# Performance work log

Measured on AMD Instinct MI355X. Metric: run time of the kernel, lower is better.

## Reference

```python
import jax, jax.numpy as jnp
import numpy as np

BN_EPS = 1e-5


def setup_inputs() -> dict:
    key = jax.random.key(0)
    k1, k2, k3 = jax.random.split(key, 3)
    B, C, H, W = 8, 1024, 48, 48
    Cb = 512
    x = jax.random.normal(k1, (B, C, H, W), dtype=jnp.float32)
    Wg = jax.random.normal(k2, (Cb, C), dtype=jnp.float32) * (1.0 / np.sqrt(C))
    Wz = jax.random.normal(k3, (C, Cb), dtype=jnp.float32) * (1.0 / np.sqrt(Cb))
    gamma = jnp.zeros((C,), dtype=jnp.float32)  # BN weight, const-init 0
    beta = jnp.zeros((C,), dtype=jnp.float32)   # BN bias,  const-init 0
    return {"x": x, "Wg": Wg, "Wz": Wz, "gamma": gamma, "beta": beta}


def reference(x, Wg, Wz, gamma, beta):
    B, C, H, W = x.shape
    HW = H * W
    xf = x.reshape(B, C, HW)                                  # [B,C,N]
    # attn[b,n,m] = <x[b,:,n], x[b,:,m]> / (H*W), softmax over m
    attn = jnp.einsum('bcn,bcm->bnm', xf, xf) / HW            # [B,N,N]
    attn = jax.nn.softmax(attn, axis=-1)
    # g: 1x1 conv C -> Cb (no bias)
    g = jnp.einsum('dc,bcn->bdn', Wg, xf)                     # [B,Cb,N]
    # y[b,d,n] = sum_m attn[b,n,m] * g[b,d,m]
    y = jnp.einsum('bnm,bdm->bdn', attn, g)                   # [B,Cb,N]
    # W_z: 1x1 conv Cb -> C (no bias)
    wy = jnp.einsum('cd,bdn->bcn', Wz, y)                     # [B,C,N]
    # BatchNorm2d in training mode: batch stats over (B, N), biased variance
    mean = jnp.mean(wy, axis=(0, 2), keepdims=True)
    var = jnp.mean(jnp.square(wy - mean), axis=(0, 2), keepdims=True)
    wy_bn = (wy - mean) * jax.lax.rsqrt(var + BN_EPS)
    wy_bn = wy_bn * gamma[None, :, None] + beta[None, :, None]
    z = wy_bn.reshape(B, C, H, W) + x
    return z
```

## Files before the change

kernel.cpp:

```cpp
#include <hip/hip_runtime.h>
#include <hip/hip_bf16.h>
#include <stdint.h>


typedef __bf16 bf16;
typedef __attribute__((ext_vector_type(8))) __bf16 bf16x8;
typedef __attribute__((ext_vector_type(4))) float f32x4;

template <bool F32OUT, bool BNRED>
__global__ __launch_bounds__(256)
void gemm_bt(const bf16* __restrict__ Ag, const bf16* __restrict__ Bg,
             void* __restrict__ Dg, int K, int N,
             long long sA, long long sB, long long sD, float alpha,
             float* __restrict__ ps, float* __restrict__ pq)
{
    __shared__ char lds[32768];
    char* ldsA = lds;
    char* ldsB = lds + 16384;

    const int lane = threadIdx.x & 63;
    const int wv   = threadIdx.x >> 6;
    const int wm   = wv >> 1;
    const int wn   = wv & 1;

    const bf16* Ab = Ag + (long long)blockIdx.z * sA + (long long)blockIdx.y * 128 * K;
    const bf16* Bb = Bg + (long long)blockIdx.z * sB + (long long)blockIdx.x * 128 * K;

    f32x4 acc[4][4];
    #pragma unroll
    for (int i = 0; i < 4; ++i)
        #pragma unroll
        for (int j = 0; j < 4; ++j) {
            f32x4 z = {0.f, 0.f, 0.f, 0.f};
            acc[i][j] = z;
        }

    for (int k0 = 0; k0 < K; k0 += 64) {
        #pragma unroll
        for (int t = 0; t < 4; ++t) {
            int ch  = (wv * 4 + t) * 64 + lane;
            int row = ch >> 3;
            int cc  = (ch & 7) ^ (row & 7);
            bf16x8 va = *(const bf16x8*)(Ab + (long long)row * K + k0 + cc * 8);
            bf16x8 vb = *(const bf16x8*)(Bb + (long long)row * K + k0 + cc * 8);
            *(bf16x8*)(ldsA + ch * 16) = va;
            *(bf16x8*)(ldsB + ch * 16) = vb;
        }
        __syncthreads();

        #pragma unroll
        for (int kk = 0; kk < 64; kk += 32) {
            bf16x8 af[4], bfr[4];
            #pragma unroll
            for (int i = 0; i < 4; ++i) {
                int r = wm * 64 + i * 16 + (lane & 15);
                int c = ((kk >> 3) + (lane >> 4)) ^ (r & 7);
                af[i] = *(const bf16x8*)(ldsA + r * 128 + c * 16);
            }
            #pragma unroll
            for (int j = 0; j < 4; ++j) {
                int r = wn * 64 + j * 16 + (lane & 15);
                int c = ((kk >> 3) + (lane >> 4)) ^ (r & 7);
                bfr[j] = *(const bf16x8*)(ldsB + r * 128 + c * 16);
            }
            #pragma unroll
            for (int i = 0; i < 4; ++i)
                #pragma unroll
                for (int j = 0; j < 4; ++j)
                    acc[i][j] = __builtin_amdgcn_mfma_f32_16x16x32_bf16(af[i], bfr[j], acc[i][j], 0, 0, 0);
        }
        __syncthreads();
    }

    float* bs = (float*)lds;
    float* bq = (float*)(lds + 512);
    if (BNRED) {
        if (threadIdx.x < 128) { bs[threadIdx.x] = 0.f; bq[threadIdx.x] = 0.f; }
        __syncthreads();
    }

    const int m_base = blockIdx.y * 128 + wm * 64;
    const int n_base = blockIdx.x * 128 + wn * 64;
    float s_it[4][4], q_it[4][4];
    #pragma unroll
    for (int i = 0; i < 4; ++i) {
        #pragma unroll
        for (int t = 0; t < 4; ++t) { s_it[i][t] = 0.f; q_it[i][t] = 0.f; }
    }
    #pragma unroll
    for (int i = 0; i < 4; ++i) {
        #pragma unroll
        for (int j = 0; j < 4; ++j) {
            int col = n_base + j * 16 + (lane & 15);
            #pragma unroll
            for (int t = 0; t < 4; ++t) {
                int rowg = m_base + i * 16 + (lane >> 4) * 4 + t;
                float v = acc[i][j][t] * alpha;
                if (F32OUT) ((float*)Dg)[(long long)blockIdx.z * sD + (long long)rowg * N + col] = v;
                else        ((bf16*)Dg)[(long long)blockIdx.z * sD + (long long)rowg * N + col] = (bf16)v;
                if (BNRED) { s_it[i][t] += v; q_it[i][t] += v * v; }
            }
        }
    }

    if (BNRED) {
        #pragma unroll
        for (int i = 0; i < 4; ++i) {
            #pragma unroll
            for (int t = 0; t < 4; ++t) {
                float s = s_it[i][t], q = q_it[i][t];
                #pragma unroll
                for (int m = 1; m < 16; m <<= 1) {
                    s += __shfl_xor(s, m);
                    q += __shfl_xor(q, m);
                }
                if ((lane & 15) == 0) {
                    int cl = wm * 64 + i * 16 + (lane >> 4) * 4 + t;
                    atomicAdd(&bs[cl], s);
                    atomicAdd(&bq[cl], q);
                }
            }
        }
        __syncthreads();
        if (threadIdx.x < 128) {
            int cg = blockIdx.y * 128 + threadIdx.x;
            atomicAdd(&ps[cg], bs[threadIdx.x]);
            atomicAdd(&pq[cg], bq[threadIdx.x]);
        }
    }
}

__global__ __launch_bounds__(256)
void f32_to_bf16(const float* __restrict__ in, bf16* __restrict__ out, int n)
{
    int idx = (blockIdx.x * 256 + threadIdx.x) * 4;
    if (idx < n) {
        float4 v = *(const float4*)(in + idx);
        out[idx + 0] = (bf16)v.x;
        out[idx + 1] = (bf16)v.y;
        out[idx + 2] = (bf16)v.z;
        out[idx + 3] = (bf16)v.w;
    }
}

__global__ __launch_bounds__(256)
void zero_f32(float* __restrict__ p)
{
    p[blockIdx.x * 256 + threadIdx.x] = 0.f;
}

__global__ __launch_bounds__(256)
void transpose_f32_bf16(const float* __restrict__ x, bf16* __restrict__ xT)
{
    __shared__ bf16 tile[32][33];
    const float* xb = x + (long long)blockIdx.z * 1024 * 2304;
    bf16* xo = xT + (long long)blockIdx.z * 2304 * 1024;
    const int n0 = blockIdx.x * 32;
    const int c0 = blockIdx.y * 32;
    const int tx = threadIdx.x, ty = threadIdx.y;
    #pragma unroll
    for (int i = 0; i < 32; i += 8)
        tile[ty + i][tx] = (bf16)xb[(long long)(c0 + ty + i) * 2304 + n0 + tx];
    __syncthreads();
    #pragma unroll
    for (int i = 0; i < 32; i += 8)
        xo[(long long)(n0 + ty + i) * 1024 + c0 + tx] = tile[tx][ty + i];
}

__global__ __launch_bounds__(256)
void softmax_rows(bf16* __restrict__ S)
{
    bf16* p = S + (long long)blockIdx.x * 2304;
    const int t = threadIdx.x;
    __shared__ float red[256];

    bf16x8 v8 = *(const bf16x8*)(p + t * 8);
    float vt = (float)p[2048 + t];
    float f[8];
    float mx = vt;
    #pragma unroll
    for (int i = 0; i < 8; ++i) { f[i] = (float)v8[i]; mx = fmaxf(mx, f[i]); }

    red[t] = mx; __syncthreads();
    for (int s = 128; s > 0; s >>= 1) { if (t < s) red[t] = fmaxf(red[t], red[t + s]); __syncthreads(); }
    mx = red[0];
    __syncthreads();

    float sum = 0.f;
    #pragma unroll
    for (int i = 0; i < 8; ++i) { f[i] = __expf(f[i] - mx); sum += f[i]; }
    vt = __expf(vt - mx); sum += vt;

    red[t] = sum; __syncthreads();
    for (int s = 128; s > 0; s >>= 1) { if (t < s) red[t] += red[t + s]; __syncthreads(); }
    float inv = 1.0f / red[0];

    bf16x8 o;
    #pragma unroll
    for (int i = 0; i < 8; ++i) o[i] = (bf16)(f[i] * inv);
    *(bf16x8*)(p + t * 8) = o;
    p[2048 + t] = (bf16)(vt * inv);
}

__global__ __launch_bounds__(256)
void bn_finalize(const float* __restrict__ ps, const float* __restrict__ pq,
                 float* __restrict__ mean, float* __restrict__ istd)
{
    int c = blockIdx.x * 256 + threadIdx.x;
    float mu = ps[c] / 18432.0f;
    mean[c] = mu;
    istd[c] = rsqrtf(pq[c] / 18432.0f - mu * mu + 1e-5f);
}

__global__ __launch_bounds__(256)
void bn_apply(const float* __restrict__ wy, const float* __restrict__ x,
              const float* __restrict__ gamma, const float* __restrict__ beta,
              const float* __restrict__ mean, const float* __restrict__ istd,
              float* __restrict__ z)
{
    long long idx = ((long long)blockIdx.x * 256 + threadIdx.x) * 4;
    int c = (int)((idx / 2304) & 1023);
    float sc = gamma[c] * istd[c];
    float sh = beta[c] - mean[c] * sc;
    float4 w  = *(const float4*)(wy + idx);
    float4 xv = *(const float4*)(x + idx);
    float4 o;
    o.x = w.x * sc + sh + xv.x;
    o.y = w.y * sc + sh + xv.y;
    o.z = w.z * sc + sh + xv.z;
    o.w = w.w * sc + sh + xv.w;
    *(float4*)(z + idx) = o;
}

extern "C" void kernel_launch(void* const* d_in, const int* in_sizes, int n_in,
                              void* d_out, int out_size, void* d_ws, size_t ws_size,
                              hipStream_t stream)
{
    const float* x     = (const float*)d_in[0];
    const float* Wg    = (const float*)d_in[1];
    const float* Wz    = (const float*)d_in[2];
    const float* gamma = (const float*)d_in[3];
    const float* beta  = (const float*)d_in[4];
    float* zo = (float*)d_out;

    const int B = 8, C = 1024, Cb = 512, N = 2304;

    const size_t fixedB = ((size_t)Cb * C * 2) * 2 + (size_t)C * 4 * 4 + 4096;
    const size_t perB   = ((size_t)N * C + (size_t)Cb * N + (size_t)N * N + (size_t)N * Cb) * 2 + 1024;
    int BC = 8;
    while (BC > 1 && fixedB + perB * (size_t)BC > ws_size) BC >>= 1;

    char* p = (char*)d_ws;
    auto alloc = [&](size_t bytes) { char* r = p; p += (bytes + 255) & ~(size_t)255; return r; };
    bf16*  Wgb  = (bf16*)alloc((size_t)Cb * C * 2);
    bf16*  Wzb  = (bf16*)alloc((size_t)C * Cb * 2);
    float* psum = (float*)alloc((size_t)C * 4);
    float* pqsm = (float*)alloc((size_t)C * 4);
    float* mean = (float*)alloc((size_t)C * 4);
    float* istd = (float*)alloc((size_t)C * 4);
    bf16*  xT   = (bf16*)alloc((size_t)BC * N * C * 2);
    bf16*  g    = (bf16*)alloc((size_t)BC * Cb * N * 2);
    bf16*  attn = (bf16*)alloc((size_t)BC * N * N * 2);
    bf16*  yT   = (bf16*)alloc((size_t)BC * N * Cb * 2);

    f32_to_bf16<<<dim3((Cb * C) / (256 * 4)), 256, 0, stream>>>(Wg, Wgb, Cb * C);
    f32_to_bf16<<<dim3((C * Cb) / (256 * 4)), 256, 0, stream>>>(Wz, Wzb, C * Cb);
    zero_f32<<<dim3(8), 256, 0, stream>>>(psum);

    for (int cs = 0; cs < B; cs += BC) {
        const float* xc = x + (long long)cs * C * N;
        float* wyc = zo + (long long)cs * C * N;

        transpose_f32_bf16<<<dim3(N / 32, C / 32, BC), dim3(32, 8), 0, stream>>>(xc, xT);

        gemm_bt<false, false><<<dim3(N / 128, Cb / 128, BC), 256, 0, stream>>>(
            Wgb, xT, g, C, N, 0, (long long)N * C, (long long)Cb * N, 1.0f, nullptr, nullptr);

        gemm_bt<false, false><<<dim3(N / 128, N / 128, BC), 256, 0, stream>>>(
            xT, xT, attn, C, N, (long long)N * C, (long long)N * C, (long long)N * N, 1.0f / 2304.0f,
            nullptr, nullptr);

        softmax_rows<<<dim3(BC * N), 256, 0, stream>>>(attn);

        gemm_bt<false, false><<<dim3(Cb / 128, N / 128, BC), 256, 0, stream>>>(
            attn, g, yT, N, Cb, (long long)N * N, (long long)Cb * N, (long long)N * Cb, 1.0f,
            nullptr, nullptr);

        gemm_bt<true, true><<<dim3(N / 128, C / 128, BC), 256, 0, stream>>>(
            Wzb, yT, wyc, Cb, N, 0, (long long)N * Cb, (long long)C * N, 1.0f, psum, pqsm);
    }

    bn_finalize<<<dim3(C / 256), 256, 0, stream>>>(psum, pqsm, mean, istd);
    bn_apply<<<dim3((B * C * N) / (256 * 4)), 256, 0, stream>>>(zo, x, gamma, beta, mean, istd, zo);
}
```

Baseline: 447.2 us.

## Prefetch next K tile into registers and reorder grid to batch-major

```diff
diff --git a/kernel.cpp b/kernel.cpp
--- a/kernel.cpp
+++ b/kernel.cpp
@@ -23,8 +23,12 @@
     const int wm   = wv >> 1;
     const int wn   = wv & 1;
 
-    const bf16* Ab = Ag + (long long)blockIdx.z * sA + (long long)blockIdx.y * 128 * K;
-    const bf16* Bb = Bg + (long long)blockIdx.z * sB + (long long)blockIdx.x * 128 * K;
+    const int zb = blockIdx.x;
+    const int bx = blockIdx.y;
+    const int by = blockIdx.z;
+
+    const bf16* Ab = Ag + (long long)zb * sA + (long long)by * 128 * K;
+    const bf16* Bb = Bg + (long long)zb * sB + (long long)bx * 128 * K;
 
     f32x4 acc[4][4];
     #pragma unroll
@@ -35,19 +39,20 @@
             acc[i][j] = z;
         }
 
-    for (int k0 = 0; k0 < K; k0 += 64) {
-        #pragma unroll
-        for (int t = 0; t < 4; ++t) {
-            int ch  = (wv * 4 + t) * 64 + lane;
-            int row = ch >> 3;
-            int cc  = (ch & 7) ^ (row & 7);
-            bf16x8 va = *(const bf16x8*)(Ab + (long long)row * K + k0 + cc * 8);
-            bf16x8 vb = *(const bf16x8*)(Bb + (long long)row * K + k0 + cc * 8);
-            *(bf16x8*)(ldsA + ch * 16) = va;
-            *(bf16x8*)(ldsB + ch * 16) = vb;
-        }
-        __syncthreads();
-
+    const bf16* gA[4];
+    const bf16* gB[4];
+    int ldsOff[4];
+    #pragma unroll
+    for (int t = 0; t < 4; ++t) {
+        int ch  = (wv * 4 + t) * 64 + lane;
+        int row = ch >> 3;
+        int cc  = (ch & 7) ^ (row & 7);
+        gA[t] = Ab + (long long)row * K + cc * 8;
+        gB[t] = Bb + (long long)row * K + cc * 8;
+        ldsOff[t] = ch * 16;
+    }
+
+    auto compute = [&]() {
         #pragma unroll
         for (int kk = 0; kk < 64; kk += 32) {
             bf16x8 af[4], bfr[4];
@@ -69,6 +74,41 @@
                 for (int j = 0; j < 4; ++j)
                     acc[i][j] = __builtin_amdgcn_mfma_f32_16x16x32_bf16(af[i], bfr[j], acc[i][j], 0, 0, 0);
         }
+    };
+
+    bf16x8 ra[4], rb[4], rc[4], rd[4];
+    #pragma unroll
+    for (int t = 0; t < 4; ++t) { ra[t] = *(const bf16x8*)(gA[t]); rb[t] = *(const bf16x8*)(gB[t]); }
+
+    for (int k0 = 0; k0 < K; k0 += 128) {
+        #pragma unroll
+        for (int t = 0; t < 4; ++t) {
+            *(bf16x8*)(ldsA + ldsOff[t]) = ra[t];
+            *(bf16x8*)(ldsB + ldsOff[t]) = rb[t];
+        }
+        #pragma unroll
+        for (int t = 0; t < 4; ++t) {
+            rc[t] = *(const bf16x8*)(gA[t] + k0 + 64);
+            rd[t] = *(const bf16x8*)(gB[t] + k0 + 64);
+        }
+        __syncthreads();
+        compute();
+        __syncthreads();
+
+        #pragma unroll
+        for (int t = 0; t < 4; ++t) {
+            *(bf16x8*)(ldsA + ldsOff[t]) = rc[t];
+            *(bf16x8*)(ldsB + ldsOff[t]) = rd[t];
+        }
+        if (k0 + 128 < K) {
+            #pragma unroll
+            for (int t = 0; t < 4; ++t) {
+                ra[t] = *(const bf16x8*)(gA[t] + k0 + 128);
+                rb[t] = *(const bf16x8*)(gB[t] + k0 + 128);
+            }
+        }
+        __syncthreads();
+        compute();
         __syncthreads();
     }
 
@@ -79,8 +119,8 @@
         __syncthreads();
     }
 
-    const int m_base = blockIdx.y * 128 + wm * 64;
-    const int n_base = blockIdx.x * 128 + wn * 64;
+    const int m_base = by * 128 + wm * 64;
+    const int n_base = bx * 128 + wn * 64;
     float s_it[4][4], q_it[4][4];
     #pragma unroll
     for (int i = 0; i < 4; ++i) {
@@ -96,8 +136,8 @@
             for (int t = 0; t < 4; ++t) {
                 int rowg = m_base + i * 16 + (lane >> 4) * 4 + t;
                 float v = acc[i][j][t] * alpha;
-                if (F32OUT) ((float*)Dg)[(long long)blockIdx.z * sD + (long long)rowg * N + col] = v;
-                else        ((bf16*)Dg)[(long long)blockIdx.z * sD + (long long)rowg * N + col] = (bf16)v;
+                if (F32OUT) ((float*)Dg)[(long long)zb * sD + (long long)rowg * N + col] = v;
+                else        ((bf16*)Dg)[(long long)zb * sD + (long long)rowg * N + col] = (bf16)v;
                 if (BNRED) { s_it[i][t] += v; q_it[i][t] += v * v; }
             }
         }
@@ -123,7 +163,7 @@
         }
         __syncthreads();
         if (threadIdx.x < 128) {
-            int cg = blockIdx.y * 128 + threadIdx.x;
+            int cg = by * 128 + threadIdx.x;
             atomicAdd(&ps[cg], bs[threadIdx.x]);
             atomicAdd(&pq[cg], bq[threadIdx.x]);
         }
@@ -273,20 +313,20 @@
 
         transpose_f32_bf16<<<dim3(N / 32, C / 32, BC), dim3(32, 8), 0, stream>>>(xc, xT);
 
-        gemm_bt<false, false><<<dim3(N / 128, Cb / 128, BC), 256, 0, stream>>>(
+        gemm_bt<false, false><<<dim3(BC, N / 128, Cb / 128), 256, 0, stream>>>(
             Wgb, xT, g, C, N, 0, (long long)N * C, (long long)Cb * N, 1.0f, nullptr, nullptr);
 
-        gemm_bt<false, false><<<dim3(N / 128, N / 128, BC), 256, 0, stream>>>(
+        gemm_bt<false, false><<<dim3(BC, N / 128, N / 128), 256, 0, stream>>>(
             xT, xT, attn, C, N, (long long)N * C, (long long)N * C, (long long)N * N, 1.0f / 2304.0f,
             nullptr, nullptr);
 
         softmax_rows<<<dim3(BC * N), 256, 0, stream>>>(attn);
 
-        gemm_bt<false, false><<<dim3(Cb / 128, N / 128, BC), 256, 0, stream>>>(
+        gemm_bt<false, false><<<dim3(BC, Cb / 128, N / 128), 256, 0, stream>>>(
             attn, g, yT, N, Cb, (long long)N * N, (long long)Cb * N, (long long)N * Cb, 1.0f,
             nullptr, nullptr);
 
-        gemm_bt<true, true><<<dim3(N / 128, C / 128, BC), 256, 0, stream>>>(
+        gemm_bt<true, true><<<dim3(BC, N / 128, C / 128), 256, 0, stream>>>(
             Wzb, yT, wyc, Cb, N, 0, (long long)N * Cb, (long long)C * N, 1.0f, psum, pqsm);
     }
 
```

Result: no change. 450.4 us (+0.7%).

## Widen GEMM tiles to 128x256 and put batch index on grid x

Applied to the files above, without the earlier changes.

```diff
diff --git a/kernel.cpp b/kernel.cpp
--- a/kernel.cpp
+++ b/kernel.cpp
@@ -14,7 +14,7 @@
              long long sA, long long sB, long long sD, float alpha,
              float* __restrict__ ps, float* __restrict__ pq)
 {
-    __shared__ char lds[32768];
+    __shared__ char lds[49152];
     char* ldsA = lds;
     char* ldsB = lds + 16384;
 
@@ -23,14 +23,18 @@
     const int wm   = wv >> 1;
     const int wn   = wv & 1;
 
-    const bf16* Ab = Ag + (long long)blockIdx.z * sA + (long long)blockIdx.y * 128 * K;
-    const bf16* Bb = Bg + (long long)blockIdx.z * sB + (long long)blockIdx.x * 128 * K;
-
-    f32x4 acc[4][4];
+    const int zb = blockIdx.x;
+    const int bx = blockIdx.y;
+    const int by = blockIdx.z;
+
+    const bf16* Ab = Ag + (long long)zb * sA + (long long)by * 128 * K;
+    const bf16* Bb = Bg + (long long)zb * sB + (long long)bx * 256 * K;
+
+    f32x4 acc[4][8];
     #pragma unroll
     for (int i = 0; i < 4; ++i)
         #pragma unroll
-        for (int j = 0; j < 4; ++j) {
+        for (int j = 0; j < 8; ++j) {
             f32x4 z = {0.f, 0.f, 0.f, 0.f};
             acc[i][j] = z;
         }
@@ -38,19 +42,23 @@
     for (int k0 = 0; k0 < K; k0 += 64) {
         #pragma unroll
         for (int t = 0; t < 4; ++t) {
-            int ch  = (wv * 4 + t) * 64 + lane;
+            int ch  = t * 256 + threadIdx.x;
             int row = ch >> 3;
             int cc  = (ch & 7) ^ (row & 7);
-            bf16x8 va = *(const bf16x8*)(Ab + (long long)row * K + k0 + cc * 8);
-            bf16x8 vb = *(const bf16x8*)(Bb + (long long)row * K + k0 + cc * 8);
-            *(bf16x8*)(ldsA + ch * 16) = va;
-            *(bf16x8*)(ldsB + ch * 16) = vb;
+            *(bf16x8*)(ldsA + ch * 16) = *(const bf16x8*)(Ab + (long long)row * K + k0 + cc * 8);
+        }
+        #pragma unroll
+        for (int t = 0; t < 8; ++t) {
+            int ch  = t * 256 + threadIdx.x;
+            int row = ch >> 3;
+            int cc  = (ch & 7) ^ (row & 7);
+            *(bf16x8*)(ldsB + ch * 16) = *(const bf16x8*)(Bb + (long long)row * K + k0 + cc * 8);
         }
         __syncthreads();
 
         #pragma unroll
         for (int kk = 0; kk < 64; kk += 32) {
-            bf16x8 af[4], bfr[4];
+            bf16x8 af[4];
             #pragma unroll
             for (int i = 0; i < 4; ++i) {
                 int r = wm * 64 + i * 16 + (lane & 15);
@@ -58,16 +66,14 @@
                 af[i] = *(const bf16x8*)(ldsA + r * 128 + c * 16);
             }
             #pragma unroll
-            for (int j = 0; j < 4; ++j) {
-                int r = wn * 64 + j * 16 + (lane & 15);
+            for (int j = 0; j < 8; ++j) {
+                int r = wn * 128 + j * 16 + (lane & 15);
                 int c = ((kk >> 3) + (lane >> 4)) ^ (r & 7);
-                bfr[j] = *(const bf16x8*)(ldsB + r * 128 + c * 16);
+                bf16x8 bfr = *(const bf16x8*)(ldsB + r * 128 + c * 16);
+                #pragma unroll
+                for (int i = 0; i < 4; ++i)
+                    acc[i][j] = __builtin_amdgcn_mfma_f32_16x16x32_bf16(af[i], bfr, acc[i][j], 0, 0, 0);
             }
-            #pragma unroll
-            for (int i = 0; i < 4; ++i)
-                #pragma unroll
-                for (int j = 0; j < 4; ++j)
-                    acc[i][j] = __builtin_amdgcn_mfma_f32_16x16x32_bf16(af[i], bfr[j], acc[i][j], 0, 0, 0);
         }
         __syncthreads();
     }
@@ -79,8 +85,8 @@
         __syncthreads();
     }
 
-    const int m_base = blockIdx.y * 128 + wm * 64;
-    const int n_base = blockIdx.x * 128 + wn * 64;
+    const int m_base = by * 128 + wm * 64;
+    const int n_base = bx * 256 + wn * 128;
     float s_it[4][4], q_it[4][4];
     #pragma unroll
     for (int i = 0; i < 4; ++i) {
@@ -90,14 +96,14 @@
     #pragma unroll
     for (int i = 0; i < 4; ++i) {
         #pragma unroll
-        for (int j = 0; j < 4; ++j) {
+        for (int j = 0; j < 8; ++j) {
             int col = n_base + j * 16 + (lane & 15);
             #pragma unroll
             for (int t = 0; t < 4; ++t) {
                 int rowg = m_base + i * 16 + (lane >> 4) * 4 + t;
                 float v = acc[i][j][t] * alpha;
-                if (F32OUT) ((float*)Dg)[(long long)blockIdx.z * sD + (long long)rowg * N + col] = v;
-                else        ((bf16*)Dg)[(long long)blockIdx.z * sD + (long long)rowg * N + col] = (bf16)v;
+                if (F32OUT) ((float*)Dg)[(long long)zb * sD + (long long)rowg * N + col] = v;
+                else        ((bf16*)Dg)[(long long)zb * sD + (long long)rowg * N + col] = (bf16)v;
                 if (BNRED) { s_it[i][t] += v; q_it[i][t] += v * v; }
             }
         }
@@ -123,7 +129,7 @@
         }
         __syncthreads();
         if (threadIdx.x < 128) {
-            int cg = blockIdx.y * 128 + threadIdx.x;
+            int cg = by * 128 + threadIdx.x;
             atomicAdd(&ps[cg], bs[threadIdx.x]);
             atomicAdd(&pq[cg], bq[threadIdx.x]);
         }
@@ -273,20 +279,20 @@
 
         transpose_f32_bf16<<<dim3(N / 32, C / 32, BC), dim3(32, 8), 0, stream>>>(xc, xT);
 
-        gemm_bt<false, false><<<dim3(N / 128, Cb / 128, BC), 256, 0, stream>>>(
+        gemm_bt<false, false><<<dim3(BC, N / 256, Cb / 128), 256, 0, stream>>>(
             Wgb, xT, g, C, N, 0, (long long)N * C, (long long)Cb * N, 1.0f, nullptr, nullptr);
 
-        gemm_bt<false, false><<<dim3(N / 128, N / 128, BC), 256, 0, stream>>>(
+        gemm_bt<false, false><<<dim3(BC, N / 256, N / 128), 256, 0, stream>>>(
             xT, xT, attn, C, N, (long long)N * C, (long long)N * C, (long long)N * N, 1.0f / 2304.0f,
             nullptr, nullptr);
 
         softmax_rows<<<dim3(BC * N), 256, 0, stream>>>(attn);
 
-        gemm_bt<false, false><<<dim3(Cb / 128, N / 128, BC), 256, 0, stream>>>(
+        gemm_bt<false, false><<<dim3(BC, Cb / 256, N / 128), 256, 0, stream>>>(
             attn, g, yT, N, Cb, (long long)N * N, (long long)Cb * N, (long long)N * Cb, 1.0f,
             nullptr, nullptr);
 
-        gemm_bt<true, true><<<dim3(N / 128, C / 128, BC), 256, 0, stream>>>(
+        gemm_bt<true, true><<<dim3(BC, N / 256, C / 128), 256, 0, stream>>>(
             Wzb, yT, wyc, Cb, N, 0, (long long)N * Cb, (long long)C * N, 1.0f, psum, pqsm);
     }
 
```

New measurement: 624.4 us. 1.4x slower.
